# Performance work log

Measured on AMD Instinct MI355X. Metric: run time of the kernel, lower is better.

## Reference

```python
import jax, jax.numpy as jnp
import numpy as np

DIM = 16384
NOBS = 8192
EPS = 1e-20


def _soft(v, tau):
    return jnp.sign(v) * jnp.maximum(jnp.abs(v) - tau, 0.0)


def setup_inputs() -> dict:
    key = jax.random.key(0)
    ks = jax.random.split(key, 14)
    A = jax.random.normal(ks[0], (NOBS, DIM), jnp.float32) / np.float32(np.sqrt(DIM))
    b = jax.random.normal(ks[1], (NOBS,), jnp.float32)
    x_old = jax.random.normal(ks[2], (DIM,), jnp.float32)
    # soft-threshold to get a realistic sparse iterate (nontrivial zeros mask)
    x_cur = _soft(jax.random.normal(ks[3], (DIM,), jnp.float32), 0.5)
    mu = jnp.array([0.1], jnp.float32)
    smoothness = jnp.array([10.0], jnp.float32)

    def glorot(k, shape):
        return jax.random.normal(k, shape, jnp.float32) * np.float32(np.sqrt(2.0 / (shape[0] + shape[1])))

    W_u1 = glorot(ks[4], (20, 8))
    W_u2 = glorot(ks[5], (20, 20))
    W_u3 = glorot(ks[6], (20, 20))
    W_u4 = glorot(ks[7], (2, 20))
    W_s1 = glorot(ks[8], (30, 12))
    W_s2 = glorot(ks[9], (20, 30))
    W_s3 = glorot(ks[10], (10, 20))
    W_s4 = glorot(ks[11], (8, 10))
    return dict(x_old=x_old, x_cur=x_cur, A=A, b=b, mu=mu, smoothness=smoothness,
                W_u1=W_u1, W_u2=W_u2, W_u3=W_u3, W_u4=W_u4,
                W_s1=W_s1, W_s2=W_s2, W_s3=W_s3, W_s4=W_s4)


def reference(x_old, x_cur, A, b, mu, smoothness,
              W_u1, W_u2, W_u3, W_u4, W_s1, W_s2, W_s3, W_s4):
    L = smoothness[0]
    m = mu[0]

    def smooth(x):
        r = A @ x - b
        return 0.5 * jnp.dot(r, r)

    def nonsmooth(x):
        return m * jnp.sum(jnp.abs(x))

    smooth_loss = smooth(x_cur)
    old_smooth_loss = smooth(x_old)
    nonsmooth_loss = nonsmooth(x_cur)
    old_nonsmooth_loss = nonsmooth(x_old)
    loss = smooth_loss + nonsmooth_loss
    old_loss = old_smooth_loss + old_nonsmooth_loss

    zeros = (x_cur == 0).astype(x_cur.dtype)   # mask of zero coordinates
    non_zeros = 1.0 - zeros

    # normalized difference of iterates
    diff = x_cur - x_old
    diff_norm = jnp.linalg.norm(diff)
    diff = jnp.where(diff_norm > EPS, diff / diff_norm, diff)
    diff_zero = diff * zeros
    diff_nonzero = diff * non_zeros
    diff_zero_norm = diff_norm * jnp.linalg.norm(diff_zero)
    diff_nonzero_norm = diff_norm * jnp.linalg.norm(diff_nonzero)

    # normalized gradient of smooth part at current iterate
    grad = A.T @ (A @ x_cur - b)
    grad_norm = jnp.linalg.norm(grad)
    grad = jnp.where(grad_norm > EPS, grad / grad_norm, grad)
    grad_zero = grad * zeros
    grad_nonzero = grad * non_zeros
    grad_zero_norm = grad_norm * jnp.linalg.norm(grad_zero)
    grad_nonzero_norm = grad_norm * jnp.linalg.norm(grad_nonzero)

    # proximal-gradient residual (stopping criterion)
    prox = _soft(x_cur - grad_norm * grad / L, m / L)
    stop_vec = x_cur - prox
    stop_norm = jnp.linalg.norm(stop_vec)
    stop_vec = jnp.where(stop_norm > EPS, stop_vec / stop_norm, stop_vec)
    stop_zero = stop_vec * zeros
    stop_nonzero = stop_vec * non_zeros
    stop_zero_norm = stop_norm * jnp.linalg.norm(stop_zero)
    stop_nonzero_norm = stop_norm * jnp.linalg.norm(stop_nonzero)

    feats = jnp.stack([
        m,
        jnp.log1p(old_loss) - jnp.log1p(loss),
        jnp.log1p(old_smooth_loss) - jnp.log1p(smooth_loss),
        jnp.log1p(old_nonsmooth_loss) - jnp.log1p(nonsmooth_loss),
        jnp.log1p(grad_zero_norm),
        jnp.log1p(grad_nonzero_norm),
        jnp.log1p(diff_zero_norm),
        jnp.log1p(diff_nonzero_norm),
        jnp.log1p(stop_zero_norm),
        jnp.log1p(stop_nonzero_norm),
        jnp.dot(grad_zero, diff_zero),
        jnp.dot(grad_nonzero, diff_nonzero),
    ])  # (12,)

    # step-size MLP: 12 -> 30 -> 20 -> 10 -> 8, ReLU, no bias
    h = feats
    for W in (W_s1, W_s2, W_s3):
        h = jax.nn.relu(W @ h)
    alpha = W_s4 @ h  # (8,)

    # 1x1-conv stack == channel matmul on [8, dim]
    chans = jnp.stack([
        alpha[0] * grad_zero,
        alpha[1] * grad_nonzero,
        alpha[2] * stop_zero,
        alpha[3] * stop_nonzero,
        alpha[4] * diff_zero,
        alpha[5] * diff_nonzero,
        alpha[6] * grad_nonzero * diff_nonzero,
        alpha[7] * grad_zero * diff_zero,
    ])  # (8, dim)
    h2 = chans
    for W in (W_u1, W_u2, W_u3):
        h2 = jax.nn.relu(W @ h2)
    direction = W_u4 @ h2  # (2, dim)

    dir_1 = direction[0] * zeros
    dir_2 = direction[1] * non_zeros
    update = _soft(x_cur + (dir_1 - grad_norm * grad + diff_norm * dir_2) / L, m / L)
    return update
```

## Files before the change

### kernel.cpp

```cpp
#include <hip/hip_runtime.h>
#include <math.h>

#define DIM   16384
#define NOBS  8192
#define EPSN  1e-20f

__device__ __forceinline__ float softf(float v, float tau) {
    float a = fmaxf(fabsf(v) - tau, 0.0f);
    return copysignf(a, v);
}

__device__ __forceinline__ float dot4(float4 a, float4 b) {
    return a.x * b.x + a.y * b.y + a.z * b.z + a.w * b.w;
}

__device__ __forceinline__ float sum16(const float* p) {
    const float4* q = (const float4*)p;
    float4 s0 = q[0], s1 = q[1], s2 = q[2], s3 = q[3];
    float a = (s0.x + s0.y) + (s0.z + s0.w);
    float b = (s1.x + s1.y) + (s1.z + s1.w);
    float c = (s2.x + s2.y) + (s2.z + s2.w);
    float d = (s3.x + s3.y) + (s3.z + s3.w);
    return (a + b) + (c + d);
}

#define DPP_ADD(x, CTRL, RM, BM)                                               \
    ((x) + __builtin_bit_cast(float, __builtin_amdgcn_update_dpp(             \
               0, __builtin_bit_cast(int, (x)), (CTRL), (RM), (BM), false)))

__device__ __forceinline__ float wave_sum64(float x) {
    x = DPP_ADD(x, 0x111, 0xF, 0xF);
    x = DPP_ADD(x, 0x112, 0xF, 0xF);
    x = DPP_ADD(x, 0x114, 0xF, 0xF);
    x = DPP_ADD(x, 0x118, 0xF, 0xF);
    x = DPP_ADD(x, 0x142, 0xA, 0xF);
    x = DPP_ADD(x, 0x143, 0xC, 0xF);
    return x;
}

__global__ __launch_bounds__(1024) void k1_fused(
    const float* __restrict__ A, const float* __restrict__ xc,
    const float* __restrict__ xo, const float* __restrict__ b,
    float* __restrict__ ws_gp,
    float* __restrict__ ws_sc)
{
    const int t   = threadIdx.x;
    const int bid = blockIdx.x;
    __shared__ __align__(16) float redc[2][16];
    __shared__ __align__(16) float redo[2][16];
    __shared__ float bsh[32];

    const int row0 = bid * 32;
    if (t < 32) bsh[t] = b[row0 + t];

    const float4* xc4 = (const float4*)xc;
    const float4* xo4 = (const float4*)xo;

    float4 xcq[4], xoq[4], gpq[4];
#pragma unroll
    for (int k = 0; k < 4; ++k) {
        xcq[k] = xc4[k * 1024 + t];
        xoq[k] = xo4[k * 1024 + t];
        gpq[k] = make_float4(0.f, 0.f, 0.f, 0.f);
    }

    const float4* Abase = (const float4*)A + (size_t)row0 * (DIM / 4);
    float4 acur[4], anxt[4];
#pragma unroll
    for (int k = 0; k < 4; ++k) acur[k] = Abase[k * 1024 + t];

    float sum_r2 = 0.f, sum_ro2 = 0.f;
    __syncthreads();

    for (int r = 0; r < 32; ++r) {
        if (r < 31) {
            const float4* An = Abase + (size_t)(r + 1) * (DIM / 4);
#pragma unroll
            for (int k = 0; k < 4; ++k) anxt[k] = An[k * 1024 + t];
        }

        float dc = 0.f, dn = 0.f;
#pragma unroll
        for (int k = 0; k < 4; ++k) {
            dc += dot4(acur[k], xcq[k]);
            dn += dot4(acur[k], xoq[k]);
        }
        dc = wave_sum64(dc);
        dn = wave_sum64(dn);
        if ((t & 63) == 63) {
            redc[r & 1][t >> 6] = dc;
            redo[r & 1][t >> 6] = dn;
        }
        __syncthreads();

        float rc = sum16(redc[r & 1]) - bsh[r];
        if (t == 0) sum_r2 += rc * rc;
        if (t == 1) {
            float ro = sum16(redo[r & 1]) - bsh[r];
            sum_ro2 += ro * ro;
        }
#pragma unroll
        for (int k = 0; k < 4; ++k) {
            gpq[k].x += acur[k].x * rc;
            gpq[k].y += acur[k].y * rc;
            gpq[k].z += acur[k].z * rc;
            gpq[k].w += acur[k].w * rc;
        }
        if (r < 31) {
#pragma unroll
            for (int k = 0; k < 4; ++k) acur[k] = anxt[k];
        }
    }

    float4* gp4 = (float4*)(ws_gp + (size_t)bid * DIM);
#pragma unroll
    for (int k = 0; k < 4; ++k) gp4[k * 1024 + t] = gpq[k];
    if (t == 0) ws_sc[bid * 2 + 0] = sum_r2;
    if (t == 1) ws_sc[bid * 2 + 1] = sum_ro2;
}

__global__ __launch_bounds__(1024) void k2_fused(
    const float* __restrict__ ws_gp, const float* __restrict__ xc,
    const float* __restrict__ xo, const float* __restrict__ mu,
    const float* __restrict__ sm,
    float* __restrict__ grad, float* __restrict__ ws_red)
{
    const int t = threadIdx.x;
    const int s = t >> 6;
    const int c = t & 63;
    const int j0 = blockIdx.x * 64;

    __shared__ float sums[16][64];

    const float* base = ws_gp + (size_t)(s * 16) * DIM + j0 + c;
    float a0 = 0.f, a1 = 0.f, a2 = 0.f, a3 = 0.f;
#pragma unroll
    for (int i = 0; i < 4; ++i) {
        a0 += base[(size_t)(4 * i + 0) * DIM];
        a1 += base[(size_t)(4 * i + 1) * DIM];
        a2 += base[(size_t)(4 * i + 2) * DIM];
        a3 += base[(size_t)(4 * i + 3) * DIM];
    }
    sums[s][c] = (a0 + a1) + (a2 + a3);
    __syncthreads();

    if (t < 64) {
        const int jj = j0 + t;
        float g = 0.f;
#pragma unroll
        for (int ss = 0; ss < 16; ++ss) g += sums[ss][t];
        grad[jj] = g;

        const float x  = xc[jj];
        const float xv = xo[jj];
        const float z  = (x == 0.f) ? 1.f : 0.f;
        const float nz = 1.f - z;
        const float d  = x - xv;
        const float m = mu[0], L = sm[0];
        const float invL = 1.f / L;
        const float pv = softf(x - g * invL, m * invL);
        const float sv = x - pv;

        float vals[10];
        vals[0] = g * g * z;
        vals[1] = g * g * nz;
        vals[2] = d * d * z;
        vals[3] = d * d * nz;
        vals[4] = g * d * z;
        vals[5] = g * d * nz;
        vals[6] = fabsf(x);
        vals[7] = fabsf(xv);
        vals[8] = sv * sv * z;
        vals[9] = sv * sv * nz;

#pragma unroll
        for (int k = 0; k < 10; ++k) {
#pragma unroll
            for (int off = 32; off > 0; off >>= 1)
                vals[k] += __shfl_down(vals[k], off);
        }
        if (t == 0) {
#pragma unroll
            for (int k = 0; k < 10; ++k) ws_red[blockIdx.x * 10 + k] = vals[k];
        }
    }
}

__global__ __launch_bounds__(256) void k34_update(
    const float* __restrict__ ws_sc,
    const float* __restrict__ ws_red,
    const float* __restrict__ grad, const float* __restrict__ xc,
    const float* __restrict__ xo, const float* __restrict__ mu,
    const float* __restrict__ sm,
    const float* __restrict__ Ws1, const float* __restrict__ Ws2,
    const float* __restrict__ Ws3, const float* __restrict__ Ws4,
    const float* __restrict__ Wu1, const float* __restrict__ Wu2,
    const float* __restrict__ Wu3, const float* __restrict__ Wu4,
    float* __restrict__ out)
{
    __shared__ float w1[160], w2[400], w3[400], w4[40];
    __shared__ float sred[4][12];
    __shared__ float feats[12];
    __shared__ float ba[32], bb[32];
    __shared__ float alpha_sh[12];

    const int t = threadIdx.x;
    for (int i = t; i < 160; i += 256) w1[i] = Wu1[i];
    for (int i = t; i < 400; i += 256) w2[i] = Wu2[i];
    for (int i = t; i < 400; i += 256) w3[i] = Wu3[i];
    if (t < 40) w4[t] = Wu4[t];

    float v[12];
    v[0] = ws_sc[2 * t + 0];
    v[1] = ws_sc[2 * t + 1];
#pragma unroll
    for (int k = 0; k < 10; ++k) v[2 + k] = ws_red[t * 10 + k];
#pragma unroll
    for (int k = 0; k < 12; ++k) {
#pragma unroll
        for (int off = 32; off > 0; off >>= 1) v[k] += __shfl_down(v[k], off);
    }
    if ((t & 63) == 0) {
#pragma unroll
        for (int k = 0; k < 12; ++k) sred[t >> 6][k] = v[k];
    }
    __syncthreads();

    if (t == 0) {
        float r[12];
#pragma unroll
        for (int k = 0; k < 12; ++k)
            r[k] = (sred[0][k] + sred[1][k]) + (sred[2][k] + sred[3][k]);
        const float sum_r2 = r[0], sum_ro2 = r[1];
        const float gz2 = r[2], gnz2 = r[3], dz2 = r[4], dnz2 = r[5];
        const float gdz = r[6], gdnz = r[7], sxc = r[8], sxo = r[9];
        const float svz2 = r[10], svnz2 = r[11];

        const float grad_norm = sqrtf(gz2 + gnz2);
        const float diff_norm = sqrtf(dz2 + dnz2);
        const float stop_norm = sqrtf(svz2 + svnz2);
        const float m = mu[0];
        float smooth = 0.5f * sum_r2, old_smooth = 0.5f * sum_ro2;
        float nonsm = m * sxc, old_nonsm = m * sxo;
        float loss = smooth + nonsm, old_loss = old_smooth + old_nonsm;

        float fg = (grad_norm > EPSN) ? 1.f / grad_norm : 1.f;
        float fd = (diff_norm > EPSN) ? 1.f / diff_norm : 1.f;
        float fs = (stop_norm > EPSN) ? 1.f / stop_norm : 1.f;

        feats[0]  = m;
        feats[1]  = log1pf(old_loss) - log1pf(loss);
        feats[2]  = log1pf(old_smooth) - log1pf(smooth);
        feats[3]  = log1pf(old_nonsm) - log1pf(nonsm);
        feats[4]  = log1pf(grad_norm * fg * sqrtf(gz2));
        feats[5]  = log1pf(grad_norm * fg * sqrtf(gnz2));
        feats[6]  = log1pf(diff_norm * fd * sqrtf(dz2));
        feats[7]  = log1pf(diff_norm * fd * sqrtf(dnz2));
        feats[8]  = log1pf(stop_norm * fs * sqrtf(svz2));
        feats[9]  = log1pf(stop_norm * fs * sqrtf(svnz2));
        feats[10] = gdz  * fg * fd;
        feats[11] = gdnz * fg * fd;
        alpha_sh[8]  = grad_norm;
        alpha_sh[9]  = diff_norm;
        alpha_sh[10] = stop_norm;
    }
    __syncthreads();

    if (t < 30) {
        float s0 = 0.f;
#pragma unroll
        for (int k = 0; k < 12; ++k) s0 += Ws1[t * 12 + k] * feats[k];
        ba[t] = fmaxf(s0, 0.f);
    }
    __syncthreads();
    if (t < 20) {
        float s0 = 0.f;
#pragma unroll
        for (int k = 0; k < 30; ++k) s0 += Ws2[t * 30 + k] * ba[k];
        bb[t] = fmaxf(s0, 0.f);
    }
    __syncthreads();
    if (t < 10) {
        float s0 = 0.f;
#pragma unroll
        for (int k = 0; k < 20; ++k) s0 += Ws3[t * 20 + k] * bb[k];
        ba[t] = fmaxf(s0, 0.f);
    }
    __syncthreads();
    if (t < 8) {
        float s0 = 0.f;
#pragma unroll
        for (int k = 0; k < 10; ++k) s0 += Ws4[t * 10 + k] * ba[k];
        alpha_sh[t] = s0;
    }
    __syncthreads();

    const int j = blockIdx.x * 256 + t;
    const float m = mu[0], L = sm[0];
    const float invL = 1.f / L;
    const float gn = alpha_sh[8], dn = alpha_sh[9], sn = alpha_sh[10];
    float a[8];
#pragma unroll
    for (int k = 0; k < 8; ++k) a[k] = alpha_sh[k];

    const float g  = grad[j];
    const float x  = xc[j];
    const float xv = xo[j];
    const float z  = (x == 0.f) ? 1.f : 0.f;
    const float nz = 1.f - z;

    const float fg = (gn > EPSN) ? 1.f / gn : 1.f;
    const float fd = (dn > EPSN) ? 1.f / dn : 1.f;
    const float fs = (sn > EPSN) ? 1.f / sn : 1.f;
    const float gg = (gn > EPSN) ? g : gn * g;

    const float pv = softf(x - gg * invL, m * invL);
    const float sv = x - pv;

    const float gN = g * fg;
    const float dN = (x - xv) * fd;
    const float sN = sv * fs;

    float ch[8];
    ch[0] = a[0] * gN * z;
    ch[1] = a[1] * gN * nz;
    ch[2] = a[2] * sN * z;
    ch[3] = a[3] * sN * nz;
    ch[4] = a[4] * dN * z;
    ch[5] = a[5] * dN * nz;
    ch[6] = a[6] * (gN * nz) * (dN * nz);
    ch[7] = a[7] * (gN * z) * (dN * z);

    float h1[20];
#pragma unroll
    for (int i = 0; i < 20; ++i) {
        float s0 = 0.f;
#pragma unroll
        for (int k = 0; k < 8; ++k) s0 += w1[i * 8 + k] * ch[k];
        h1[i] = fmaxf(s0, 0.f);
    }
    float h2[20];
#pragma unroll
    for (int i = 0; i < 20; ++i) {
        float s0 = 0.f;
#pragma unroll
        for (int k = 0; k < 20; ++k) s0 += w2[i * 20 + k] * h1[k];
        h2[i] = fmaxf(s0, 0.f);
    }
    float h3[20];
#pragma unroll
    for (int i = 0; i < 20; ++i) {
        float s0 = 0.f;
#pragma unroll
        for (int k = 0; k < 20; ++k) s0 += w3[i * 20 + k] * h2[k];
        h3[i] = fmaxf(s0, 0.f);
    }
    float d0 = 0.f, d1 = 0.f;
#pragma unroll
    for (int k = 0; k < 20; ++k) {
        d0 += w4[k] * h3[k];
        d1 += w4[20 + k] * h3[k];
    }

    const float dir1 = d0 * z;
    const float dir2 = d1 * nz;
    const float arg  = x + (dir1 - gg + dn * dir2) * invL;
    out[j] = softf(arg, m * invL);
}

extern "C" void kernel_launch(void* const* d_in, const int* in_sizes, int n_in,
                              void* d_out, int out_size, void* d_ws, size_t ws_size,
                              hipStream_t stream)
{
    const float* x_old = (const float*)d_in[0];
    const float* x_cur = (const float*)d_in[1];
    const float* A     = (const float*)d_in[2];
    const float* b     = (const float*)d_in[3];
    const float* mu    = (const float*)d_in[4];
    const float* sm    = (const float*)d_in[5];
    const float* Wu1   = (const float*)d_in[6];
    const float* Wu2   = (const float*)d_in[7];
    const float* Wu3   = (const float*)d_in[8];
    const float* Wu4   = (const float*)d_in[9];
    const float* Ws1   = (const float*)d_in[10];
    const float* Ws2   = (const float*)d_in[11];
    const float* Ws3   = (const float*)d_in[12];
    const float* Ws4   = (const float*)d_in[13];
    float* out = (float*)d_out;

    float* ws      = (float*)d_ws;
    float* ws_gp   = ws;
    float* ws_sc   = ws_gp  + (size_t)256 * DIM;
    float* ws_red  = ws_sc  + 512;
    float* ws_grad = ws_red + 2560;

    k1_fused  <<<256, 1024, 0, stream>>>(A, x_cur, x_old, b, ws_gp, ws_sc);
    k2_fused  <<<256, 1024, 0, stream>>>(ws_gp, x_cur, x_old, mu, sm, ws_grad, ws_red);
    k34_update<<<64,  256,  0, stream>>>(ws_sc, ws_red, ws_grad, x_cur, x_old, mu, sm,
                                         Ws1, Ws2, Ws3, Ws4, Wu1, Wu2, Wu3, Wu4, out);
}
```

Before: 118.4 us.

## Stream A rows through LDS with async global_load_lds double buffering

```diff
diff --git a/kernel.cpp b/kernel.cpp
--- a/kernel.cpp
+++ b/kernel.cpp
@@ -1,5 +1,6 @@
 #include <hip/hip_runtime.h>
 #include <math.h>
+#include <stdint.h>
 
 #define DIM   16384
 #define NOBS  8192
@@ -38,6 +39,15 @@
     return x;
 }
 
+__device__ __forceinline__ void gload16(const float* g, float* l) {
+    __builtin_amdgcn_global_load_lds(
+        reinterpret_cast<const __attribute__((address_space(1))) void*>(
+            reinterpret_cast<uintptr_t>(g)),
+        reinterpret_cast<__attribute__((address_space(3))) void*>(
+            reinterpret_cast<uintptr_t>(l)),
+        16, 0, 0);
+}
+
 __global__ __launch_bounds__(1024) void k1_fused(
     const float* __restrict__ A, const float* __restrict__ xc,
     const float* __restrict__ xo, const float* __restrict__ b,
@@ -46,6 +56,8 @@
 {
     const int t   = threadIdx.x;
     const int bid = blockIdx.x;
+
+    __shared__ __align__(16) float abuf[2][DIM];
     __shared__ __align__(16) float redc[2][16];
     __shared__ __align__(16) float redo[2][16];
     __shared__ float bsh[32];
@@ -55,7 +67,6 @@
 
     const float4* xc4 = (const float4*)xc;
     const float4* xo4 = (const float4*)xo;
-
     float4 xcq[4], xoq[4], gpq[4];
 #pragma unroll
     for (int k = 0; k < 4; ++k) {
@@ -63,35 +74,50 @@
         xoq[k] = xo4[k * 1024 + t];
         gpq[k] = make_float4(0.f, 0.f, 0.f, 0.f);
     }
-
-    const float4* Abase = (const float4*)A + (size_t)row0 * (DIM / 4);
-    float4 acur[4], anxt[4];
-#pragma unroll
-    for (int k = 0; k < 4; ++k) acur[k] = Abase[k * 1024 + t];
+    __syncthreads();
+
+    const int woff = __builtin_amdgcn_readfirstlane((t >> 6) << 8);
+    const float* Ab = A + (size_t)row0 * DIM;
+
+#define STAGE_ROW(GROW, LBUF)                                                  \
+    do {                                                                       \
+        _Pragma("unroll")                                                      \
+        for (int k = 0; k < 4; ++k)                                            \
+            gload16((GROW) + (k << 12) + 4 * t, (LBUF) + (k << 12) + woff);    \
+    } while (0)
+
+    STAGE_ROW(Ab, abuf[0]);
+    STAGE_ROW(Ab + DIM, abuf[1]);
 
     float sum_r2 = 0.f, sum_ro2 = 0.f;
-    __syncthreads();
 
     for (int r = 0; r < 32; ++r) {
-        if (r < 31) {
-            const float4* An = Abase + (size_t)(r + 1) * (DIM / 4);
-#pragma unroll
-            for (int k = 0; k < 4; ++k) anxt[k] = An[k * 1024 + t];
-        }
-
-        float dc = 0.f, dn = 0.f;
-#pragma unroll
-        for (int k = 0; k < 4; ++k) {
-            dc += dot4(acur[k], xcq[k]);
-            dn += dot4(acur[k], xoq[k]);
-        }
+        if (r < 31) asm volatile("s_waitcnt vmcnt(4)" ::: "memory");
+        else        asm volatile("s_waitcnt vmcnt(0)" ::: "memory");
+        __builtin_amdgcn_sched_barrier(0);
+
+        const float4* ab4 = (const float4*)abuf[r & 1];
+        float4 a0 = ab4[t];
+        float4 a1 = ab4[1024 + t];
+        float4 a2 = ab4[2048 + t];
+        float4 a3 = ab4[3072 + t];
+        asm volatile("s_waitcnt lgkmcnt(0)" ::: "memory");
+        __builtin_amdgcn_sched_barrier(0);
+        if (r + 2 < 32) STAGE_ROW(Ab + (size_t)(r + 2) * DIM, abuf[r & 1]);
+
+        float dc = dot4(a0, xcq[0]); dc += dot4(a1, xcq[1]);
+        dc += dot4(a2, xcq[2]);      dc += dot4(a3, xcq[3]);
+        float dn = dot4(a0, xoq[0]); dn += dot4(a1, xoq[1]);
+        dn += dot4(a2, xoq[2]);      dn += dot4(a3, xoq[3]);
         dc = wave_sum64(dc);
         dn = wave_sum64(dn);
         if ((t & 63) == 63) {
             redc[r & 1][t >> 6] = dc;
             redo[r & 1][t >> 6] = dn;
         }
-        __syncthreads();
+        asm volatile("s_waitcnt lgkmcnt(0)" ::: "memory");
+        __builtin_amdgcn_s_barrier();
+        asm volatile("" ::: "memory");
 
         float rc = sum16(redc[r & 1]) - bsh[r];
         if (t == 0) sum_r2 += rc * rc;
@@ -99,22 +125,22 @@
             float ro = sum16(redo[r & 1]) - bsh[r];
             sum_ro2 += ro * ro;
         }
-#pragma unroll
-        for (int k = 0; k < 4; ++k) {
-            gpq[k].x += acur[k].x * rc;
-            gpq[k].y += acur[k].y * rc;
-            gpq[k].z += acur[k].z * rc;
-            gpq[k].w += acur[k].w * rc;
-        }
-        if (r < 31) {
-#pragma unroll
-            for (int k = 0; k < 4; ++k) acur[k] = anxt[k];
-        }
-    }
+        gpq[0].x += a0.x * rc; gpq[0].y += a0.y * rc;
+        gpq[0].z += a0.z * rc; gpq[0].w += a0.w * rc;
+        gpq[1].x += a1.x * rc; gpq[1].y += a1.y * rc;
+        gpq[1].z += a1.z * rc; gpq[1].w += a1.w * rc;
+        gpq[2].x += a2.x * rc; gpq[2].y += a2.y * rc;
+        gpq[2].z += a2.z * rc; gpq[2].w += a2.w * rc;
+        gpq[3].x += a3.x * rc; gpq[3].y += a3.y * rc;
+        gpq[3].z += a3.z * rc; gpq[3].w += a3.w * rc;
+    }
+#undef STAGE_ROW
 
     float4* gp4 = (float4*)(ws_gp + (size_t)bid * DIM);
-#pragma unroll
-    for (int k = 0; k < 4; ++k) gp4[k * 1024 + t] = gpq[k];
+    gp4[t]        = gpq[0];
+    gp4[1024 + t] = gpq[1];
+    gp4[2048 + t] = gpq[2];
+    gp4[3072 + t] = gpq[3];
     if (t == 0) ws_sc[bid * 2 + 0] = sum_r2;
     if (t == 1) ws_sc[bid * 2 + 1] = sum_ro2;
 }
```

New measurement: 119.4 us. Within noise of the previous version (+0.8%).

## Process two A rows per iteration, move x_old to LDS, use raw barrier

Applied to the files above, without the earlier changes.

```diff
diff --git a/kernel.cpp b/kernel.cpp
--- a/kernel.cpp
+++ b/kernel.cpp
@@ -1,5 +1,6 @@
 #include <hip/hip_runtime.h>
 #include <math.h>
+#include <stdint.h>
 
 #define DIM   16384
 #define NOBS  8192
@@ -46,69 +47,99 @@
 {
     const int t   = threadIdx.x;
     const int bid = blockIdx.x;
-    __shared__ __align__(16) float redc[2][16];
-    __shared__ __align__(16) float redo[2][16];
+
+    __shared__ __align__(16) float xos[DIM + 5120];
+    __shared__ __align__(16) float redc[2][2][16];
+    __shared__ __align__(16) float redo[2][2][16];
     __shared__ float bsh[32];
 
     const int row0 = bid * 32;
     if (t < 32) bsh[t] = b[row0 + t];
 
-    const float4* xc4 = (const float4*)xc;
-    const float4* xo4 = (const float4*)xo;
-
-    float4 xcq[4], xoq[4], gpq[4];
+    const float4* xc4  = (const float4*)xc;
+    const float4* xo4g = (const float4*)xo;
+    float4* xos4w = (float4*)xos;
+
+    float4 xcq[4], gpq[4];
 #pragma unroll
     for (int k = 0; k < 4; ++k) {
         xcq[k] = xc4[k * 1024 + t];
-        xoq[k] = xo4[k * 1024 + t];
+        xos4w[k * 1024 + t] = xo4g[k * 1024 + t];
         gpq[k] = make_float4(0.f, 0.f, 0.f, 0.f);
     }
 
-    const float4* Abase = (const float4*)A + (size_t)row0 * (DIM / 4);
-    float4 acur[4], anxt[4];
-#pragma unroll
-    for (int k = 0; k < 4; ++k) acur[k] = Abase[k * 1024 + t];
-
+    const float4* Ab = (const float4*)(A + (size_t)row0 * DIM);
+    float4 a0q[4], a1q[4], n0q[4], n1q[4];
+#pragma unroll
+    for (int k = 0; k < 4; ++k) a0q[k] = Ab[k * 1024 + t];
+#pragma unroll
+    for (int k = 0; k < 4; ++k) a1q[k] = Ab[4096 + k * 1024 + t];
+
+    __syncthreads();
+
+    const float4* xos4 = (const float4*)xos;
     float sum_r2 = 0.f, sum_ro2 = 0.f;
-    __syncthreads();
-
-    for (int r = 0; r < 32; ++r) {
-        if (r < 31) {
-            const float4* An = Abase + (size_t)(r + 1) * (DIM / 4);
-#pragma unroll
-            for (int k = 0; k < 4; ++k) anxt[k] = An[k * 1024 + t];
-        }
-
-        float dc = 0.f, dn = 0.f;
+
+    for (int i = 0; i < 16; ++i) {
+        const int r   = 2 * i;
+        const int par = i & 1;
+
+        if (i < 15) {
+            const float4* An = Ab + (size_t)(r + 2) * 4096;
+#pragma unroll
+            for (int k = 0; k < 4; ++k) n0q[k] = An[k * 1024 + t];
+#pragma unroll
+            for (int k = 0; k < 4; ++k) n1q[k] = An[4096 + k * 1024 + t];
+        }
+
+        float bv0 = bsh[r], bv1 = bsh[r + 1];
+
+        float dc0 = 0.f, dc1 = 0.f, dn0 = 0.f, dn1 = 0.f;
 #pragma unroll
         for (int k = 0; k < 4; ++k) {
-            dc += dot4(acur[k], xcq[k]);
-            dn += dot4(acur[k], xoq[k]);
-        }
-        dc = wave_sum64(dc);
-        dn = wave_sum64(dn);
+            float4 xov = xos4[k * 1024 + t];
+            dc0 += dot4(a0q[k], xcq[k]);
+            dc1 += dot4(a1q[k], xcq[k]);
+            dn0 += dot4(a0q[k], xov);
+            dn1 += dot4(a1q[k], xov);
+        }
+        dc0 = wave_sum64(dc0);
+        dc1 = wave_sum64(dc1);
+        dn0 = wave_sum64(dn0);
+        dn1 = wave_sum64(dn1);
         if ((t & 63) == 63) {
-            redc[r & 1][t >> 6] = dc;
-            redo[r & 1][t >> 6] = dn;
-        }
-        __syncthreads();
-
-        float rc = sum16(redc[r & 1]) - bsh[r];
-        if (t == 0) sum_r2 += rc * rc;
+            const int w = t >> 6;
+            redc[par][0][w] = dc0;
+            redc[par][1][w] = dc1;
+            redo[par][0][w] = dn0;
+            redo[par][1][w] = dn1;
+        }
+        asm volatile("s_waitcnt lgkmcnt(0)" ::: "memory");
+        __builtin_amdgcn_s_barrier();
+        asm volatile("" ::: "memory");
+
+        const float rc0 = sum16(redc[par][0]) - bv0;
+        const float rc1 = sum16(redc[par][1]) - bv1;
+        if (t == 0) {
+            sum_r2 += rc0 * rc0;
+            sum_r2 += rc1 * rc1;
+        }
         if (t == 1) {
-            float ro = sum16(redo[r & 1]) - bsh[r];
-            sum_ro2 += ro * ro;
+            float ro0 = sum16(redo[par][0]) - bv0;
+            float ro1 = sum16(redo[par][1]) - bv1;
+            sum_ro2 += ro0 * ro0;
+            sum_ro2 += ro1 * ro1;
         }
 #pragma unroll
         for (int k = 0; k < 4; ++k) {
-            gpq[k].x += acur[k].x * rc;
-            gpq[k].y += acur[k].y * rc;
-            gpq[k].z += acur[k].z * rc;
-            gpq[k].w += acur[k].w * rc;
-        }
-        if (r < 31) {
-#pragma unroll
-            for (int k = 0; k < 4; ++k) acur[k] = anxt[k];
+            gpq[k].x += a0q[k].x * rc0 + a1q[k].x * rc1;
+            gpq[k].y += a0q[k].y * rc0 + a1q[k].y * rc1;
+            gpq[k].z += a0q[k].z * rc0 + a1q[k].z * rc1;
+            gpq[k].w += a0q[k].w * rc0 + a1q[k].w * rc1;
+        }
+        if (i < 15) {
+#pragma unroll
+            for (int k = 0; k < 4; ++k) { a0q[k] = n0q[k]; a1q[k] = n1q[k]; }
         }
     }
 
```

Result: slower. 204.9 us (+73.0%).
